# Performance work log

Hardware: AMD Instinct MI355X
Metric: run time of the kernel (lower is better)

The kernel has to match this reference:

```python
import jax, jax.numpy as jnp
import numpy as np
import itertools

K = 3          # kernel_size
STRIDE = 1
PAD = 1
CIN = 4
COUT = 8
N_ROT = 24


def _rot_index_maps(k):
    """Source voxel indices (d,h,w) for each of the 24 proper octahedral rotations.

    Equivalent to affine_grid(R) + grid_sample on the [k,k,k] kernel: for odd k
    and align_corners=False the normalized sample points coincide exactly with
    voxel centers, so trilinear interpolation reduces to index permutation.
    """
    m = (k - 1) // 2
    mats = []
    for perm in itertools.permutations(range(3)):
        for signs in itertools.product([1, -1], repeat=3):
            R = np.zeros((3, 3))
            for i in range(3):
                R[i, perm[i]] = signs[i]
            if np.linalg.det(R) > 0.5:  # proper rotations only -> 24 matrices
                mats.append(R)
    c = np.arange(k) - m                       # centered voxel coords
    cz, cy, cx = np.meshgrid(c, c, c, indexing='ij')  # (d,h,w) order
    v = np.stack([cx, cy, cz], 0).astype(np.float64)  # (3,k,k,k) in (x,y,z)
    idx = []
    for R in mats:
        g = np.einsum('ij,jdhw->idhw', R, v)   # sampling coords (gx,gy,gz)
        idx.append(np.stack([g[2] + m, g[1] + m, g[0] + m], 0).round().astype(np.int64))
    return np.stack(idx, 0)  # (24, 3, k, k, k) source (d,h,w) indices

_IDX = _rot_index_maps(K)
IDX_D = jnp.asarray(_IDX[:, 0])
IDX_H = jnp.asarray(_IDX[:, 1])
IDX_W = jnp.asarray(_IDX[:, 2])


def setup_inputs() -> dict:
    key = jax.random.key(0)
    k1, k2, k3 = jax.random.split(key, 3)
    x = jax.random.normal(k1, (2, CIN, 64, 64, 64), dtype=jnp.float32)
    fan_in = CIN * K ** 3
    bound = (6.0 / ((1.0 + 5.0) * fan_in)) ** 0.5  # kaiming_uniform, a=sqrt(5)
    weight = jax.random.uniform(k2, (COUT, CIN, K, K, K), dtype=jnp.float32,
                                minval=-bound, maxval=bound)
    bias = jax.random.normal(k3, (COUT,), dtype=jnp.float32) * 0.01
    return {"x": x, "weight": weight, "bias": bias}


def reference(x, weight, bias):
    O, I = weight.shape[0], weight.shape[1]
    # Rotated filter bank: gather -> (O, I, 24, K, K, K) -> (24*O, I, K, K, K)
    wr = weight[:, :, IDX_D, IDX_H, IDX_W]
    wr = jnp.transpose(wr, (2, 0, 1, 3, 4, 5)).reshape(N_ROT * O, I, K, K, K)
    y = jax.lax.conv_general_dilated(
        x, wr,
        window_strides=(STRIDE,) * 3,
        padding=[(PAD, PAD)] * 3,
        dimension_numbers=('NCDHW', 'OIDHW', 'NCDHW'))
    n, _, d, h, w = y.shape
    y = y.reshape(n, N_ROT, O, d, h, w)
    y = y + bias[None, None, :, None, None, None]
    return y
```

## Files before the change

kernel.cpp:

```cpp
#include <hip/hip_runtime.h>
#include <cstdint>
#include <cstddef>

typedef __attribute__((ext_vector_type(8))) short short8;
typedef __attribute__((ext_vector_type(4))) float f32x4;
typedef __attribute__((ext_vector_type(4))) unsigned int u32x4;

#define NROT 24
#define COUT 8
#define CIN  4
#define M_TOT 192
#define PLANE 262144
#define XD 3
#define XH 6
#define XW 66

__device__ __forceinline__ unsigned short f2bf(float f) {
  unsigned u = __builtin_bit_cast(unsigned, f);
  return (unsigned short)((u + 0x7FFFu + ((u >> 16) & 1u)) >> 16);
}

__device__ __forceinline__ void rot_mat(int r, int Rm[3][3]) {
  const int perms[6][3] = {{0,1,2},{0,2,1},{1,0,2},{1,2,0},{2,0,1},{2,1,0}};
  const int psign[6] = {1,-1,-1,1,1,-1};
  int count = 0;
  for (int pe = 0; pe < 6; ++pe)
    for (int si = 0; si < 8; ++si) {
      const int s0 = (si & 4) ? -1 : 1;
      const int s1 = (si & 2) ? -1 : 1;
      const int s2 = (si & 1) ? -1 : 1;
      if (psign[pe] * s0 * s1 * s2 > 0) {
        if (count == r) {
          for (int a = 0; a < 3; ++a)
            for (int b = 0; b < 3; ++b) Rm[a][b] = 0;
          Rm[0][perms[pe][0]] = s0;
          Rm[1][perms[pe][1]] = s1;
          Rm[2][perms[pe][2]] = s2;
          return;
        }
        ++count;
      }
    }
}

__global__ void prep_A(const float* __restrict__ weight, unsigned short* __restrict__ Abuf) {
  const int tid = threadIdx.x;
  for (int ent = tid; ent < 12 * 4 * 64; ent += 256) {
    const int lane = ent & 63;
    const int mc = ent >> 6;
    const int Mtile = mc >> 2, chunk = mc & 3;
    const int m = Mtile * 16 + (lane & 15);
    const int r = m >> 3, o = m & 7;
    int Rm[3][3];
    rot_mat(r, Rm);
    unsigned short v8[8];
#pragma unroll
    for (int e = 0; e < 8; ++e) {
      const int k = chunk * 32 + (lane >> 4) * 8 + e;
      unsigned short hv = 0;
      if (k < 108) {
        const int t = k >> 2, i = k & 3;
        const int kd = t / 9, kh = (t / 3) % 3, kw = t % 3;
        const int cx = kw - 1, cy = kh - 1, cz = kd - 1;
        const int g0 = Rm[0][0] * cx + Rm[0][1] * cy + Rm[0][2] * cz;
        const int g1 = Rm[1][0] * cx + Rm[1][1] * cy + Rm[1][2] * cz;
        const int g2 = Rm[2][0] * cx + Rm[2][1] * cy + Rm[2][2] * cz;
        const int sd = g2 + 1, sh = g1 + 1, sw = g0 + 1;
        hv = f2bf(weight[(o * CIN + i) * 27 + sd * 9 + sh * 3 + sw]);
      }
      v8[e] = hv;
    }
    u32x4 packed;
    packed.x = (unsigned)v8[0] | ((unsigned)v8[1] << 16);
    packed.y = (unsigned)v8[2] | ((unsigned)v8[3] << 16);
    packed.z = (unsigned)v8[4] | ((unsigned)v8[5] << 16);
    packed.w = (unsigned)v8[6] | ((unsigned)v8[7] << 16);
    ((u32x4*)Abuf)[ent] = packed;
  }
}

__global__ __launch_bounds__(256)
void conv_mfma(const float* __restrict__ xin,
               const unsigned short* __restrict__ Abuf,
               const float* __restrict__ bias,
               float* __restrict__ out) {
  __shared__ uint2 xsv[XD * XH * XW];
  __shared__ float obuf[4][4][4][68];

  const int tid = threadIdx.x;
  int bid = blockIdx.x;
  const int ht = bid & 15; bid >>= 4;
  const int d  = bid & 63; bid >>= 6;
  const int n  = bid;
  const int h0 = ht * 4;

  const float* xb = xin + (size_t)n * CIN * PLANE;
  for (int v = tid; v < XD * XH * XW; v += 256) {
    const int ww = v % XW;
    const int rest = v / XW;
    const int yy = rest % XH;
    const int zz = rest / XH;
    const int gz = d - 1 + zz, gy = h0 - 1 + yy, gw = ww - 1;
    unsigned p0 = 0, p1 = 0;
    if ((unsigned)gz < 64u && (unsigned)gy < 64u && (unsigned)gw < 64u) {
      const int base = gz * 4096 + gy * 64 + gw;
      const unsigned a0 = f2bf(xb[base]);
      const unsigned a1 = f2bf(xb[base + PLANE]);
      const unsigned a2 = f2bf(xb[base + 2 * PLANE]);
      const unsigned a3 = f2bf(xb[base + 3 * PLANE]);
      p0 = a0 | (a1 << 16);
      p1 = a2 | (a3 << 16);
    }
    xsv[v] = make_uint2(p0, p1);
  }

  const int wv = tid >> 6;
  const int lane = tid & 63;
  const int lg = lane >> 4;
  const int col = lane & 15;

  const float bv = bias[col & 7];

  int voff[4][2];
#pragma unroll
  for (int c = 0; c < 4; ++c)
#pragma unroll
    for (int hf = 0; hf < 2; ++hf) {
      int t = c * 8 + lg * 2 + hf;
      t = t > 26 ? 26 : t;
      const int kd = t / 9, kh = (t / 3) % 3, kw = t % 3;
      voff[c][hf] = (kd * XH + kh) * XW + col + kw;
    }

  __syncthreads();

  const int nbase = n * M_TOT;
  const int wv3 = wv * 3;
  const short8* Ab8 = (const short8*)Abuf;
  const int spb = d * 4096 + h0 * 64;

#pragma unroll 1
  for (int j = 0; j < 3; ++j) {
    short8 af[4];
#pragma unroll
    for (int c = 0; c < 4; ++c)
      af[c] = Ab8[((wv3 + j) * 4 + c) * 64 + lane];

    f32x4 acc16[16];
#pragma unroll
    for (int hh = 0; hh < 4; ++hh) {
#pragma unroll
      for (int q = 0; q < 4; ++q) {
        const int dl = hh * XW + q * 16;
        f32x4 acc = {bv, bv, bv, bv};
#pragma unroll
        for (int c = 0; c < 4; ++c) {
          const uint2 lo = xsv[voff[c][0] + dl];
          const uint2 hi = xsv[voff[c][1] + dl];
          u32x4 bw;
          bw.x = lo.x; bw.y = lo.y; bw.z = hi.x; bw.w = hi.y;
          const short8 b = __builtin_bit_cast(short8, bw);
          acc = __builtin_amdgcn_mfma_f32_16x16x32_bf16(b, af[c], acc, 0, 0, 0);
        }
        acc16[hh * 4 + q] = acc;
      }
    }

#pragma unroll
    for (int g = 0; g < 4; ++g) {
      if ((col >> 2) == g) {
#pragma unroll
        for (int hq = 0; hq < 16; ++hq)
          *(f32x4*)&obuf[wv][col & 3][hq >> 2][(hq & 3) * 16 + lg * 4] = acc16[hq];
      }
      __builtin_amdgcn_sched_barrier(0);
      asm volatile("s_waitcnt lgkmcnt(0)" ::: "memory");
      __builtin_amdgcn_sched_barrier(0);
#pragma unroll
      for (int cc = 0; cc < 4; ++cc) {
        const f32x4 v = *(const f32x4*)&obuf[wv][cc][lane >> 4][(lane & 15) * 4];
        const int ch = g * 4 + cc;
        float* p = out + (size_t)(nbase + (wv3 + j) * 16 + ch) * PLANE + spb + lane * 4;
        *(f32x4*)p = v;
      }
      __builtin_amdgcn_sched_barrier(0);
      asm volatile("s_waitcnt lgkmcnt(0)" ::: "memory");
      __builtin_amdgcn_sched_barrier(0);
    }
  }
}

extern "C" void kernel_launch(void* const* d_in, const int* in_sizes, int n_in,
                              void* d_out, int out_size, void* d_ws, size_t ws_size,
                              hipStream_t stream) {
  const float* x = (const float*)d_in[0];
  const float* w = (const float*)d_in[1];
  const float* b = (const float*)d_in[2];
  float* out = (float*)d_out;
  unsigned short* Abuf = (unsigned short*)d_ws;

  prep_A<<<dim3(1), dim3(256), 0, stream>>>(w, Abuf);
  conv_mfma<<<dim3(2048), dim3(256), 0, stream>>>(x, Abuf, b, out);
}
```

Baseline: 111.4 us.

## Split accumulator into halves, double-buffer epilogue LDS, parallelize weight prep

The conv kernel now computes and stores output in two halves of 8 accumulators instead of 16, which cuts register pressure and may allow higher occupancy. The epilogue LDS staging buffer is double-buffered by group parity, so the trailing wait after each group's global stores is dropped. Stores become 8-byte instead of 16-byte vectors. The weight-prep kernel is spread over 12 blocks instead of looping in one block, shortening that serial launch.

```diff
diff --git a/kernel.cpp b/kernel.cpp
--- a/kernel.cpp
+++ b/kernel.cpp
@@ -4,6 +4,7 @@
 
 typedef __attribute__((ext_vector_type(8))) short short8;
 typedef __attribute__((ext_vector_type(4))) float f32x4;
+typedef __attribute__((ext_vector_type(2))) float f32x2;
 typedef __attribute__((ext_vector_type(4))) unsigned int u32x4;
 
 #define NROT 24
@@ -44,39 +45,38 @@
 }
 
 __global__ void prep_A(const float* __restrict__ weight, unsigned short* __restrict__ Abuf) {
-  const int tid = threadIdx.x;
-  for (int ent = tid; ent < 12 * 4 * 64; ent += 256) {
-    const int lane = ent & 63;
-    const int mc = ent >> 6;
-    const int Mtile = mc >> 2, chunk = mc & 3;
-    const int m = Mtile * 16 + (lane & 15);
-    const int r = m >> 3, o = m & 7;
-    int Rm[3][3];
-    rot_mat(r, Rm);
-    unsigned short v8[8];
-#pragma unroll
-    for (int e = 0; e < 8; ++e) {
-      const int k = chunk * 32 + (lane >> 4) * 8 + e;
-      unsigned short hv = 0;
-      if (k < 108) {
-        const int t = k >> 2, i = k & 3;
-        const int kd = t / 9, kh = (t / 3) % 3, kw = t % 3;
-        const int cx = kw - 1, cy = kh - 1, cz = kd - 1;
-        const int g0 = Rm[0][0] * cx + Rm[0][1] * cy + Rm[0][2] * cz;
-        const int g1 = Rm[1][0] * cx + Rm[1][1] * cy + Rm[1][2] * cz;
-        const int g2 = Rm[2][0] * cx + Rm[2][1] * cy + Rm[2][2] * cz;
-        const int sd = g2 + 1, sh = g1 + 1, sw = g0 + 1;
-        hv = f2bf(weight[(o * CIN + i) * 27 + sd * 9 + sh * 3 + sw]);
-      }
-      v8[e] = hv;
-    }
-    u32x4 packed;
-    packed.x = (unsigned)v8[0] | ((unsigned)v8[1] << 16);
-    packed.y = (unsigned)v8[2] | ((unsigned)v8[3] << 16);
-    packed.z = (unsigned)v8[4] | ((unsigned)v8[5] << 16);
-    packed.w = (unsigned)v8[6] | ((unsigned)v8[7] << 16);
-    ((u32x4*)Abuf)[ent] = packed;
+  const int ent = blockIdx.x * 256 + threadIdx.x;
+  if (ent >= 12 * 4 * 64) return;
+  const int lane = ent & 63;
+  const int mc = ent >> 6;
+  const int Mtile = mc >> 2, chunk = mc & 3;
+  const int m = Mtile * 16 + (lane & 15);
+  const int r = m >> 3, o = m & 7;
+  int Rm[3][3];
+  rot_mat(r, Rm);
+  unsigned short v8[8];
+#pragma unroll
+  for (int e = 0; e < 8; ++e) {
+    const int k = chunk * 32 + (lane >> 4) * 8 + e;
+    unsigned short hv = 0;
+    if (k < 108) {
+      const int t = k >> 2, i = k & 3;
+      const int kd = t / 9, kh = (t / 3) % 3, kw = t % 3;
+      const int cx = kw - 1, cy = kh - 1, cz = kd - 1;
+      const int g0 = Rm[0][0] * cx + Rm[0][1] * cy + Rm[0][2] * cz;
+      const int g1 = Rm[1][0] * cx + Rm[1][1] * cy + Rm[1][2] * cz;
+      const int g2 = Rm[2][0] * cx + Rm[2][1] * cy + Rm[2][2] * cz;
+      const int sd = g2 + 1, sh = g1 + 1, sw = g0 + 1;
+      hv = f2bf(weight[(o * CIN + i) * 27 + sd * 9 + sh * 3 + sw]);
+    }
+    v8[e] = hv;
   }
+  u32x4 packed;
+  packed.x = (unsigned)v8[0] | ((unsigned)v8[1] << 16);
+  packed.y = (unsigned)v8[2] | ((unsigned)v8[3] << 16);
+  packed.z = (unsigned)v8[4] | ((unsigned)v8[5] << 16);
+  packed.w = (unsigned)v8[6] | ((unsigned)v8[7] << 16);
+  ((u32x4*)Abuf)[ent] = packed;
 }
 
 __global__ __launch_bounds__(256)
@@ -85,7 +85,7 @@
                const float* __restrict__ bias,
                float* __restrict__ out) {
   __shared__ uint2 xsv[XD * XH * XW];
-  __shared__ float obuf[4][4][4][68];
+  __shared__ float obuf[4][2][4][2][68];
 
   const int tid = threadIdx.x;
   int bid = blockIdx.x;
@@ -146,11 +146,13 @@
     for (int c = 0; c < 4; ++c)
       af[c] = Ab8[((wv3 + j) * 4 + c) * 64 + lane];
 
-    f32x4 acc16[16];
-#pragma unroll
-    for (int hh = 0; hh < 4; ++hh) {
-#pragma unroll
-      for (int q = 0; q < 4; ++q) {
+#pragma unroll 1
+    for (int half = 0; half < 2; ++half) {
+      f32x4 acc8[8];
+#pragma unroll
+      for (int hq = 0; hq < 8; ++hq) {
+        const int hh = half * 2 + (hq >> 2);
+        const int q = hq & 3;
         const int dl = hh * XW + q * 16;
         f32x4 acc = {bv, bv, bv, bv};
 #pragma unroll
@@ -162,30 +164,29 @@
           const short8 b = __builtin_bit_cast(short8, bw);
           acc = __builtin_amdgcn_mfma_f32_16x16x32_bf16(b, af[c], acc, 0, 0, 0);
         }
-        acc16[hh * 4 + q] = acc;
+        acc8[hq] = acc;
       }
-    }
-
-#pragma unroll
-    for (int g = 0; g < 4; ++g) {
-      if ((col >> 2) == g) {
-#pragma unroll
-        for (int hq = 0; hq < 16; ++hq)
-          *(f32x4*)&obuf[wv][col & 3][hq >> 2][(hq & 3) * 16 + lg * 4] = acc16[hq];
+
+#pragma unroll
+      for (int g = 0; g < 4; ++g) {
+        const int par = g & 1;
+        if ((col >> 2) == g) {
+#pragma unroll
+          for (int hq = 0; hq < 8; ++hq)
+            *(f32x4*)&obuf[wv][par][col & 3][hq >> 2][(hq & 3) * 16 + lg * 4] = acc8[hq];
+        }
+        __builtin_amdgcn_sched_barrier(0);
+        asm volatile("s_waitcnt lgkmcnt(0)" ::: "memory");
+        __builtin_amdgcn_sched_barrier(0);
+#pragma unroll
+        for (int cc = 0; cc < 4; ++cc) {
+          const f32x2 v = *(const f32x2*)&obuf[wv][par][cc][lane >> 5][(lane & 31) * 2];
+          const int ch = g * 4 + cc;
+          float* p = out + (size_t)(nbase + (wv3 + j) * 16 + ch) * PLANE
+                         + spb + half * 128 + lane * 2;
+          *(f32x2*)p = v;
+        }
       }
-      __builtin_amdgcn_sched_barrier(0);
-      asm volatile("s_waitcnt lgkmcnt(0)" ::: "memory");
-      __builtin_amdgcn_sched_barrier(0);
-#pragma unroll
-      for (int cc = 0; cc < 4; ++cc) {
-        const f32x4 v = *(const f32x4*)&obuf[wv][cc][lane >> 4][(lane & 15) * 4];
-        const int ch = g * 4 + cc;
-        float* p = out + (size_t)(nbase + (wv3 + j) * 16 + ch) * PLANE + spb + lane * 4;
-        *(f32x4*)p = v;
-      }
-      __builtin_amdgcn_sched_barrier(0);
-      asm volatile("s_waitcnt lgkmcnt(0)" ::: "memory");
-      __builtin_amdgcn_sched_barrier(0);
     }
   }
 }
@@ -199,6 +200,6 @@
   float* out = (float*)d_out;
   unsigned short* Abuf = (unsigned short*)d_ws;
 
-  prep_A<<<dim3(1), dim3(256), 0, stream>>>(w, Abuf);
+  prep_A<<<dim3(12), dim3(256), 0, stream>>>(w, Abuf);
   conv_mfma<<<dim3(2048), dim3(256), 0, stream>>>(x, Abuf, b, out);
 }
```

Measured after the change: 97.45 us. 12.5% less time.

## Stream conv output per h-row to shrink LDS/registers; parallelize weight prep

Applied to the files above, without the earlier changes.

The main kernel no longer holds all 16 accumulator tiles before writing. It now computes and writes out one h-row (4 MFMA tiles) at a time, which shrinks the LDS staging buffer fourfold and cuts accumulator register pressure to allow higher occupancy. Each staging pass now stores a 256-byte row segment per channel instead of a full 1 KB contiguous block, and the h loop is no longer unrolled. The weight-prep kernel moves from a single block to 12 blocks, one thread per entry.

```diff
diff --git a/kernel.cpp b/kernel.cpp
--- a/kernel.cpp
+++ b/kernel.cpp
@@ -44,39 +44,38 @@
 }
 
 __global__ void prep_A(const float* __restrict__ weight, unsigned short* __restrict__ Abuf) {
-  const int tid = threadIdx.x;
-  for (int ent = tid; ent < 12 * 4 * 64; ent += 256) {
-    const int lane = ent & 63;
-    const int mc = ent >> 6;
-    const int Mtile = mc >> 2, chunk = mc & 3;
-    const int m = Mtile * 16 + (lane & 15);
-    const int r = m >> 3, o = m & 7;
-    int Rm[3][3];
-    rot_mat(r, Rm);
-    unsigned short v8[8];
-#pragma unroll
-    for (int e = 0; e < 8; ++e) {
-      const int k = chunk * 32 + (lane >> 4) * 8 + e;
-      unsigned short hv = 0;
-      if (k < 108) {
-        const int t = k >> 2, i = k & 3;
-        const int kd = t / 9, kh = (t / 3) % 3, kw = t % 3;
-        const int cx = kw - 1, cy = kh - 1, cz = kd - 1;
-        const int g0 = Rm[0][0] * cx + Rm[0][1] * cy + Rm[0][2] * cz;
-        const int g1 = Rm[1][0] * cx + Rm[1][1] * cy + Rm[1][2] * cz;
-        const int g2 = Rm[2][0] * cx + Rm[2][1] * cy + Rm[2][2] * cz;
-        const int sd = g2 + 1, sh = g1 + 1, sw = g0 + 1;
-        hv = f2bf(weight[(o * CIN + i) * 27 + sd * 9 + sh * 3 + sw]);
-      }
-      v8[e] = hv;
-    }
-    u32x4 packed;
-    packed.x = (unsigned)v8[0] | ((unsigned)v8[1] << 16);
-    packed.y = (unsigned)v8[2] | ((unsigned)v8[3] << 16);
-    packed.z = (unsigned)v8[4] | ((unsigned)v8[5] << 16);
-    packed.w = (unsigned)v8[6] | ((unsigned)v8[7] << 16);
-    ((u32x4*)Abuf)[ent] = packed;
+  const int ent = blockIdx.x * 256 + threadIdx.x;
+  if (ent >= 12 * 4 * 64) return;
+  const int lane = ent & 63;
+  const int mc = ent >> 6;
+  const int Mtile = mc >> 2, chunk = mc & 3;
+  const int m = Mtile * 16 + (lane & 15);
+  const int r = m >> 3, o = m & 7;
+  int Rm[3][3];
+  rot_mat(r, Rm);
+  unsigned short v8[8];
+#pragma unroll
+  for (int e = 0; e < 8; ++e) {
+    const int k = chunk * 32 + (lane >> 4) * 8 + e;
+    unsigned short hv = 0;
+    if (k < 108) {
+      const int t = k >> 2, i = k & 3;
+      const int kd = t / 9, kh = (t / 3) % 3, kw = t % 3;
+      const int cx = kw - 1, cy = kh - 1, cz = kd - 1;
+      const int g0 = Rm[0][0] * cx + Rm[0][1] * cy + Rm[0][2] * cz;
+      const int g1 = Rm[1][0] * cx + Rm[1][1] * cy + Rm[1][2] * cz;
+      const int g2 = Rm[2][0] * cx + Rm[2][1] * cy + Rm[2][2] * cz;
+      const int sd = g2 + 1, sh = g1 + 1, sw = g0 + 1;
+      hv = f2bf(weight[(o * CIN + i) * 27 + sd * 9 + sh * 3 + sw]);
+    }
+    v8[e] = hv;
   }
+  u32x4 packed;
+  packed.x = (unsigned)v8[0] | ((unsigned)v8[1] << 16);
+  packed.y = (unsigned)v8[2] | ((unsigned)v8[3] << 16);
+  packed.z = (unsigned)v8[4] | ((unsigned)v8[5] << 16);
+  packed.w = (unsigned)v8[6] | ((unsigned)v8[7] << 16);
+  ((u32x4*)Abuf)[ent] = packed;
 }
 
 __global__ __launch_bounds__(256)
@@ -85,7 +84,7 @@
                const float* __restrict__ bias,
                float* __restrict__ out) {
   __shared__ uint2 xsv[XD * XH * XW];
-  __shared__ float obuf[4][4][4][68];
+  __shared__ float obuf[4][4][68];
 
   const int tid = threadIdx.x;
   int bid = blockIdx.x;
@@ -138,6 +137,8 @@
   const int wv3 = wv * 3;
   const short8* Ab8 = (const short8*)Abuf;
   const int spb = d * 4096 + h0 * 64;
+  const int cc = lane >> 4;
+  const int off = (lane & 15) * 4;
 
 #pragma unroll 1
   for (int j = 0; j < 3; ++j) {
@@ -146,13 +147,15 @@
     for (int c = 0; c < 4; ++c)
       af[c] = Ab8[((wv3 + j) * 4 + c) * 64 + lane];
 
-    f32x4 acc16[16];
-#pragma unroll
+    const size_t jch = (size_t)(nbase + (wv3 + j) * 16);
+
+#pragma unroll 1
     for (int hh = 0; hh < 4; ++hh) {
+      f32x4 acc[4];
 #pragma unroll
       for (int q = 0; q < 4; ++q) {
         const int dl = hh * XW + q * 16;
-        f32x4 acc = {bv, bv, bv, bv};
+        f32x4 a = {bv, bv, bv, bv};
 #pragma unroll
         for (int c = 0; c < 4; ++c) {
           const uint2 lo = xsv[voff[c][0] + dl];
@@ -160,32 +163,26 @@
           u32x4 bw;
           bw.x = lo.x; bw.y = lo.y; bw.z = hi.x; bw.w = hi.y;
           const short8 b = __builtin_bit_cast(short8, bw);
-          acc = __builtin_amdgcn_mfma_f32_16x16x32_bf16(b, af[c], acc, 0, 0, 0);
+          a = __builtin_amdgcn_mfma_f32_16x16x32_bf16(b, af[c], a, 0, 0, 0);
         }
-        acc16[hh * 4 + q] = acc;
+        acc[q] = a;
       }
-    }
-
-#pragma unroll
-    for (int g = 0; g < 4; ++g) {
-      if ((col >> 2) == g) {
-#pragma unroll
-        for (int hq = 0; hq < 16; ++hq)
-          *(f32x4*)&obuf[wv][col & 3][hq >> 2][(hq & 3) * 16 + lg * 4] = acc16[hq];
+
+#pragma unroll
+      for (int g = 0; g < 4; ++g) {
+        if ((col >> 2) == g) {
+#pragma unroll
+          for (int q = 0; q < 4; ++q)
+            *(f32x4*)&obuf[wv][col & 3][q * 16 + lg * 4] = acc[q];
+        }
+        __builtin_amdgcn_sched_barrier(0);
+        asm volatile("s_waitcnt lgkmcnt(0)" ::: "memory");
+        __builtin_amdgcn_sched_barrier(0);
+        const f32x4 v = *(const f32x4*)&obuf[wv][cc][off];
+        float* p = out + (jch + g * 4 + cc) * PLANE + spb + hh * 64 + off;
+        *(f32x4*)p = v;
+        __builtin_amdgcn_sched_barrier(0);
       }
-      __builtin_amdgcn_sched_barrier(0);
-      asm volatile("s_waitcnt lgkmcnt(0)" ::: "memory");
-      __builtin_amdgcn_sched_barrier(0);
-#pragma unroll
-      for (int cc = 0; cc < 4; ++cc) {
-        const f32x4 v = *(const f32x4*)&obuf[wv][cc][lane >> 4][(lane & 15) * 4];
-        const int ch = g * 4 + cc;
-        float* p = out + (size_t)(nbase + (wv3 + j) * 16 + ch) * PLANE + spb + lane * 4;
-        *(f32x4*)p = v;
-      }
-      __builtin_amdgcn_sched_barrier(0);
-      asm volatile("s_waitcnt lgkmcnt(0)" ::: "memory");
-      __builtin_amdgcn_sched_barrier(0);
     }
   }
 }
@@ -199,6 +196,6 @@
   float* out = (float*)d_out;
   unsigned short* Abuf = (unsigned short*)d_ws;
 
-  prep_A<<<dim3(1), dim3(256), 0, stream>>>(w, Abuf);
+  prep_A<<<dim3(12), dim3(256), 0, stream>>>(w, Abuf);
   conv_mfma<<<dim3(2048), dim3(256), 0, stream>>>(x, Abuf, b, out);
 }
```

New measurement: 89.88 us (median of 2 runs). -19.3%, faster.
